# Optimization experiments

Measured on AMD Instinct MI355X. Metric: run time of the kernel, lower is better.

Reference implementation:

```python
import jax, jax.numpy as jnp
import numpy as np

N, E = 50000, 800000
NODE_IN, EDGE_IN = 32, 16
EMB, GEMB = 128, 128
H, C, L, B = 4, 32, 2, 8   # heads, per-head dim, layers, graphs
GAT_IN = NODE_IN + EMB      # skip_conn=True
NEG_SLOPE = 0.2
EPS = 1e-5


def layernorm(x, g, b):
    m = jnp.mean(x, -1, keepdims=True)
    v = jnp.mean((x - m) ** 2, -1, keepdims=True)
    return (x - m) / jnp.sqrt(v + EPS) * g + b


def setup_inputs() -> dict:
    key = jax.random.key(0)
    ks = jax.random.split(key, 24)
    s = 0.05
    return {
        "x": jax.random.normal(ks[0], (N, NODE_IN), jnp.float32),
        "edge_attr": jax.random.normal(ks[1], (E, EDGE_IN), jnp.float32),
        "W_in": jax.random.normal(ks[2], (NODE_IN, EMB), jnp.float32) * s,
        "b_in": jnp.zeros((EMB,), jnp.float32),
        "W_src": jax.random.normal(ks[3], (L, GAT_IN, H * C), jnp.float32) * s,
        "W_edge": jax.random.normal(ks[4], (L, EDGE_IN, H * C), jnp.float32) * s,
        "att_src": jax.random.normal(ks[5], (L, H, C), jnp.float32) * s,
        "att_dst": jax.random.normal(ks[6], (L, H, C), jnp.float32) * s,
        "att_edge": jax.random.normal(ks[7], (L, H, C), jnp.float32) * s,
        "gat_bias": jnp.zeros((L, H * C), jnp.float32),
        "ln_gamma": jnp.ones((L, EMB), jnp.float32),
        "ln_beta": jnp.zeros((L, EMB), jnp.float32),
        "W_out": jax.random.normal(ks[8], (EMB, EMB), jnp.float32) * s,
        "b_out": jnp.zeros((EMB,), jnp.float32),
        "ln_out_gamma": jnp.ones((EMB,), jnp.float32),
        "ln_out_beta": jnp.zeros((EMB,), jnp.float32),
        "W_g": jax.random.normal(ks[9], (EMB, GEMB), jnp.float32) * s,
        "b_g": jnp.zeros((GEMB,), jnp.float32),
        "g_gamma": jnp.ones((GEMB,), jnp.float32),
        "g_beta": jnp.zeros((GEMB,), jnp.float32),
        "edge_index": jax.random.randint(ks[10], (2, E), 0, N, jnp.int32),
        "batch": jnp.sort(jax.random.randint(ks[11], (N,), 0, B, jnp.int32)),
    }


def reference(x, edge_attr, W_in, b_in, W_src, W_edge, att_src, att_dst, att_edge,
              gat_bias, ln_gamma, ln_beta, W_out, b_out, ln_out_gamma, ln_out_beta,
              W_g, b_g, g_gamma, g_beta, edge_index, batch):
    # PyG GATConv adds self-loops with edge_attr fill_value='mean'
    loop = jnp.arange(N, dtype=edge_index.dtype)
    src = jnp.concatenate([edge_index[0], loop])   # [E2]
    dst = jnp.concatenate([edge_index[1], loop])   # [E2]
    ea = jnp.concatenate([edge_attr, jnp.broadcast_to(edge_attr.mean(0), (N, EDGE_IN))], 0)

    h = jax.nn.relu(x @ W_in + b_in)  # [N, EMB]
    for l in range(L):
        inp = jnp.concatenate([x, h], -1)                   # skip connection [N, GAT_IN]
        xs = (inp @ W_src[l]).reshape(N, H, C)              # projected nodes
        a_s = jnp.einsum('nhc,hc->nh', xs, att_src[l])
        a_d = jnp.einsum('nhc,hc->nh', xs, att_dst[l])
        ee = (ea @ W_edge[l]).reshape(-1, H, C)             # [E2, H, C]
        a_e = jnp.einsum('ehc,hc->eh', ee, att_edge[l])
        alpha = jax.nn.leaky_relu(a_s[src] + a_d[dst] + a_e, NEG_SLOPE)  # [E2, H]
        # segment softmax over incoming edges of each destination node
        amax = jax.ops.segment_max(alpha, dst, num_segments=N)
        ex = jnp.exp(alpha - amax[dst])
        denom = jax.ops.segment_sum(ex, dst, num_segments=N)
        w = ex / (denom[dst] + 1e-16)
        msg = xs[src] * w[:, :, None]                        # [E2, H, C]
        out = jax.ops.segment_sum(msg, dst, num_segments=N).reshape(N, H * C) + gat_bias[l]
        h = jax.nn.elu(layernorm(out, ln_gamma[l], ln_beta[l]))

    g = layernorm(jax.nn.relu(h @ W_g + b_g), g_gamma, g_beta)
    gsum = jax.ops.segment_sum(g, batch, num_segments=B)
    cnt = jax.ops.segment_sum(jnp.ones((N, 1), g.dtype), batch, num_segments=B)
    graph_embeddings = gsum / jnp.maximum(cnt, 1.0)

    node_embeddings = layernorm(jax.nn.relu(h @ W_out + b_out), ln_out_gamma, ln_out_beta)
    return node_embeddings, graph_embeddings
```

## Files before the change

kernel.cpp:

```cpp
#include <hip/hip_runtime.h>

#define N_NODES 50000
#define N_EDGES 800000
#define E2      850000
#define NODE_IN 32
#define EDGE_IN 16
#define EMB     128
#define GAT_IN  160
#define NLAYER  2
#define NGRAPH  8
#define NBLK    196
#define NB32    1563
#define NB64    782

#define GWT_SRC0 0
#define GWT_SRC1 20480
#define GWT_OUT  40960
#define GWT_G    57344
#define GWT_TOT  73728

typedef short bf16x8 __attribute__((ext_vector_type(8)));
typedef float f32x4 __attribute__((ext_vector_type(4)));

__device__ __forceinline__ unsigned int f2bf(float f) {
    unsigned int u = __float_as_uint(f);
    return (u + 0x7FFFu + ((u >> 16) & 1u)) >> 16;
}
__device__ __forceinline__ float bf2f(unsigned int h) {
    return __uint_as_float(h << 16);
}
__device__ __forceinline__ unsigned int pack2bf(float a, float b) {
    return f2bf(a) | (f2bf(b) << 16);
}

__global__ void zero_kernel(float* __restrict__ p, int n) {
    int i = blockIdx.x * blockDim.x + threadIdx.x;
    int stride = gridDim.x * blockDim.x;
    for (; i < n; i += stride) p[i] = 0.f;
}

__global__ __launch_bounds__(256) void count_mean_kernel(const int* __restrict__ edge_index,
                                                         const float* __restrict__ edge_attr,
                                                         int* __restrict__ cnt4,
                                                         int* __restrict__ rank,
                                                         float* __restrict__ meta) {
    __shared__ float sm[16];
    int t = threadIdx.x;
    int e = blockIdx.x * 256 + t;
    if (e < E2) {
        int dst = (e < N_EDGES) ? edge_index[N_EDGES + e] : (e - N_EDGES);
        int shard = blockIdx.x & 3;
        rank[e] = atomicAdd(&cnt4[shard * N_NODES + dst], 1);
    }
    if (blockIdx.x < 512) {
        if (t < 16) sm[t] = 0.f;
        __syncthreads();
        int gid = blockIdx.x * 256 + t;
        int q = gid & 3;
        const float4* ea4 = (const float4*)edge_attr;
        float4 s = make_float4(0.f, 0.f, 0.f, 0.f);
        for (int j = gid; j < N_EDGES * 4; j += 512 * 256) {
            float4 v = ea4[j];
            s.x += v.x; s.y += v.y; s.z += v.z; s.w += v.w;
        }
        atomicAdd(&sm[q * 4 + 0], s.x);
        atomicAdd(&sm[q * 4 + 1], s.y);
        atomicAdd(&sm[q * 4 + 2], s.z);
        atomicAdd(&sm[q * 4 + 3], s.w);
        __syncthreads();
        if (t < 16) atomicAdd(&meta[t], sm[t]);
    }
}

__global__ void prep_kernel(const float* __restrict__ W_edge,
                            const float* __restrict__ att_edge,
                            float* __restrict__ meta) {
    int t = threadIdx.x;
    if (t < EDGE_IN) meta[t] = meta[t] * (1.0f / (float)N_EDGES);
    __syncthreads();
    {
        int l = t >> 6, k = (t >> 2) & 15, h = t & 3;
        const float* w = W_edge + ((size_t)l * EDGE_IN + k) * EMB + h * 32;
        const float* a = att_edge + (size_t)l * EMB + h * 32;
        float acc = 0.f;
#pragma unroll
        for (int c = 0; c < 32; c++) acc += w[c] * a[c];
        meta[16 + (l * 16 + k) * 4 + h] = acc;
    }
    __syncthreads();
    if (t < 8) {
        int l = t >> 2, h = t & 3;
        float acc = 0.f;
#pragma unroll
        for (int k = 0; k < EDGE_IN; k++) acc += meta[k] * meta[16 + (l * 16 + k) * 4 + h];
        meta[144 + t] = acc;
    }
}

__global__ __launch_bounds__(256) void prep_wt_kernel(const float* __restrict__ Wsrc,
                                                      const float* __restrict__ Wout,
                                                      const float* __restrict__ Wg,
                                                      unsigned short* __restrict__ gwt) {
    int g = blockIdx.x * 256 + threadIdx.x;
    const float* Wm;
    int base, gg;
    if (g < 5120) {
        int l = g / 2560;
        gg = g - l * 2560;
        Wm = Wsrc + (size_t)l * GAT_IN * EMB;
        base = l * 20480;
    } else if (g < 7168) {
        gg = g - 5120;
        Wm = Wout;
        base = GWT_OUT;
    } else {
        gg = g - 7168;
        Wm = Wg;
        base = GWT_G;
    }
    int lane = gg & 63, tmp = gg >> 6;
    int nt = tmp & 7, kc = tmp >> 3;
    int quad = lane >> 4, l16 = lane & 15;
    int col = nt * 16 + l16, k0 = kc * 32 + quad * 8;
    unsigned int u[4];
#pragma unroll
    for (int j = 0; j < 4; j++)
        u[j] = pack2bf(Wm[(size_t)(k0 + 2 * j) * EMB + col], Wm[(size_t)(k0 + 2 * j + 1) * EMB + col]);
    *(uint4*)(gwt + base + (size_t)gg * 8) = make_uint4(u[0], u[1], u[2], u[3]);
}

__global__ __launch_bounds__(256) void scan1_kernel(const int* __restrict__ cnt4,
                                                    int* __restrict__ bsum) {
    __shared__ int sm[256];
    int t = threadIdx.x;
    int i = blockIdx.x * 256 + t;
    int tot = 0;
    if (i < N_NODES) {
#pragma unroll
        for (int s = 0; s < 4; s++) tot += cnt4[s * N_NODES + i];
    }
    sm[t] = tot;
    __syncthreads();
#pragma unroll
    for (int d = 128; d >= 1; d >>= 1) {
        if (t < d) sm[t] += sm[t + d];
        __syncthreads();
    }
    if (t == 0) bsum[blockIdx.x] = sm[0];
}

__global__ __launch_bounds__(256) void scan2_kernel(const int* __restrict__ bsum,
                                                    int* __restrict__ bbase) {
    __shared__ int sm[256];
    int t = threadIdx.x;
    int v = (t < NBLK) ? bsum[t] : 0;
    sm[t] = v;
    __syncthreads();
#pragma unroll
    for (int d = 1; d < 256; d <<= 1) {
        int u = (t >= d) ? sm[t - d] : 0;
        __syncthreads();
        sm[t] += u;
        __syncthreads();
    }
    if (t < NBLK) bbase[t] = sm[t] - v;
}

__global__ __launch_bounds__(256) void scan3_kernel(const int* __restrict__ bbase,
                                                    const int* __restrict__ cnt4,
                                                    int* __restrict__ off,
                                                    int* __restrict__ shard_base) {
    __shared__ int sm[256];
    int t = threadIdx.x;
    int i = blockIdx.x * 256 + t;
    int c[4] = {0, 0, 0, 0};
    int tot = 0;
    if (i < N_NODES) {
#pragma unroll
        for (int s = 0; s < 4; s++) {
            c[s] = cnt4[s * N_NODES + i];
            tot += c[s];
        }
    }
    sm[t] = tot;
    __syncthreads();
#pragma unroll
    for (int d = 1; d < 256; d <<= 1) {
        int u = (t >= d) ? sm[t - d] : 0;
        __syncthreads();
        sm[t] += u;
        __syncthreads();
    }
    if (i < N_NODES) {
        int base = bbase[blockIdx.x] + sm[t] - tot;
        off[i] = base;
        int4 sb;
        sb.x = base;            base += c[0];
        sb.y = base;            base += c[1];
        sb.z = base;            base += c[2];
        sb.w = base;
        *(int4*)(shard_base + i * 4) = sb;
        if (i == N_NODES - 1) off[N_NODES] = E2;
    }
}

__global__ __launch_bounds__(256) void fill_perm_kernel(const int* __restrict__ edge_index,
                                                        const int* __restrict__ rank,
                                                        const int* __restrict__ shard_base,
                                                        int* __restrict__ perm) {
    int e = blockIdx.x * 256 + threadIdx.x;
    if (e >= E2) return;
    int src, dst;
    if (e < N_EDGES) {
        src = edge_index[e];
        dst = edge_index[N_EDGES + e];
    } else {
        src = dst = e - N_EDGES;
    }
    int shard = (e >> 8) & 3;
    int pos = shard_base[dst * 4 + shard] + rank[e];
    ((int2*)perm)[pos] = make_int2(src, e);
}

__global__ __launch_bounds__(256) void compute_ae_kernel(const int* __restrict__ perm,
                                                         const float* __restrict__ edge_attr,
                                                         const float* __restrict__ meta,
                                                         int* __restrict__ csr_src,
                                                         float* __restrict__ csr_ae0,
                                                         float* __restrict__ csr_ae1) {
    __shared__ float Ml[128];
    __shared__ float loop_ae[8];
    int t = threadIdx.x;
    if (t < 128) Ml[t] = meta[16 + t];
    if (t < 8) loop_ae[t] = meta[144 + t];
    __syncthreads();
    int p = blockIdx.x * 256 + t;
    if (p >= E2) return;
    int2 pe = ((const int2*)perm)[p];
    int src = pe.x, e = pe.y;
    csr_src[p] = src;
    float ae[2][4];
    if (e < N_EDGES) {
        const float4* r4 = (const float4*)(edge_attr + (size_t)e * EDGE_IN);
#pragma unroll
        for (int l = 0; l < 2; l++)
#pragma unroll
            for (int hh = 0; hh < 4; hh++) ae[l][hh] = 0.f;
#pragma unroll
        for (int q = 0; q < 4; q++) {
            float4 v = r4[q];
#pragma unroll
            for (int l = 0; l < 2; l++) {
                const float* M = Ml + l * 64;
#pragma unroll
                for (int hh = 0; hh < 4; hh++) {
                    ae[l][hh] += v.x * M[(4 * q + 0) * 4 + hh] + v.y * M[(4 * q + 1) * 4 + hh] +
                                 v.z * M[(4 * q + 2) * 4 + hh] + v.w * M[(4 * q + 3) * 4 + hh];
                }
            }
        }
    } else {
#pragma unroll
        for (int l = 0; l < 2; l++)
#pragma unroll
            for (int hh = 0; hh < 4; hh++) ae[l][hh] = loop_ae[l * 4 + hh];
    }
    *(float4*)(csr_ae0 + (size_t)p * 4) = make_float4(ae[0][0], ae[0][1], ae[0][2], ae[0][3]);
    *(float4*)(csr_ae1 + (size_t)p * 4) = make_float4(ae[1][0], ae[1][1], ae[1][2], ae[1][3]);
}

__global__ __launch_bounds__(256) void input_proj_kernel(const float* __restrict__ x,
                                                         const float* __restrict__ W,
                                                         const float* __restrict__ b,
                                                         unsigned int* __restrict__ h_bf,
                                                         unsigned int* __restrict__ x_bf) {
    __shared__ float inp[32][NODE_IN];
    int t = threadIdx.x;
    int n0 = blockIdx.x * 32;
    for (int i = t; i < 32 * NODE_IN; i += 256) {
        int r = i >> 5, c = i & 31;
        int n = min(n0 + r, N_NODES - 1);
        inp[r][c] = x[(size_t)n * NODE_IN + c];
    }
    __syncthreads();
    for (int i = t; i < 32 * 16; i += 256) {
        int r = i >> 4, c = i & 15;
        int n = n0 + r;
        if (n < N_NODES) x_bf[(size_t)n * 16 + c] = pack2bf(inp[r][2 * c], inp[r][2 * c + 1]);
    }
    int wave = t >> 6, lane = t & 63;
    int c0 = lane * 2, c1 = c0 + 1;
    const float2* W2 = (const float2*)W;
    float acc[8][2];
#pragma unroll
    for (int j = 0; j < 8; j++) { acc[j][0] = b[c0]; acc[j][1] = b[c1]; }
#pragma unroll 2
    for (int k4 = 0; k4 < NODE_IN / 4; k4++) {
        float4 v[8];
#pragma unroll
        for (int j = 0; j < 8; j++) v[j] = *(const float4*)&inp[wave * 8 + j][k4 * 4];
#pragma unroll
        for (int kk = 0; kk < 4; kk++) {
            float2 w = W2[(k4 * 4 + kk) * 64 + lane];
#pragma unroll
            for (int j = 0; j < 8; j++) {
                float vv = (&v[j].x)[kk];
                acc[j][0] += vv * w.x;
                acc[j][1] += vv * w.y;
            }
        }
    }
#pragma unroll
    for (int j = 0; j < 8; j++) {
        int n = n0 + wave * 8 + j;
        if (n < N_NODES)
            h_bf[(size_t)n * 64 + lane] = pack2bf(fmaxf(acc[j][0], 0.f), fmaxf(acc[j][1], 0.f));
    }
}

template <int K, int MODE>
__global__ __launch_bounds__(256) void dense_mfma_kernel(
    const unsigned int* __restrict__ xbf, const unsigned int* __restrict__ hbf,
    const unsigned short* __restrict__ gwt, const float* __restrict__ bias,
    const float* __restrict__ v1, const float* __restrict__ v2,
    const int* __restrict__ batch,
    unsigned int* __restrict__ xs_out, float* __restrict__ a_s, float* __restrict__ a_d,
    float* __restrict__ out_nodes, float* __restrict__ gsum, float* __restrict__ gcnt) {
    constexpr int CLS = 132;
    __shared__ __align__(16) float cl[64 * CLS];
    __shared__ float red[(MODE != 0) ? 64 : 1][8];
    __shared__ float locw[(MODE == 2) ? 4 : 1][2][EMB];
    __shared__ int bids[(MODE == 2) ? 64 : 1];

    int t = threadIdx.x;
    int n0 = blockIdx.x * 64;
    if (MODE == 2 && t < 64) bids[t] = batch[min(n0 + t, N_NODES - 1)];

    int wave = t >> 6, lane = t & 63;
    int quad = lane >> 4, l16 = lane & 15;
    int arow = min(n0 + wave * 16 + l16, N_NODES - 1);
    const bf16x8* B = (const bf16x8*)gwt;
    f32x4 acc[8];
#pragma unroll
    for (int i = 0; i < 8; i++) acc[i] = (f32x4){0.f, 0.f, 0.f, 0.f};
#pragma unroll
    for (int kc = 0; kc < K / 32; kc++) {
        bf16x8 af;
        if (MODE == 0 && kc == 0) {
            af = *(const bf16x8*)(xbf + (size_t)arow * 16 + quad * 4);
        } else {
            int hk = ((MODE == 0) ? (kc - 1) : kc) * 16;
            af = *(const bf16x8*)(hbf + (size_t)arow * 64 + hk + quad * 4);
        }
#pragma unroll
        for (int nt = 0; nt < 8; nt++) {
            bf16x8 bfv = B[(kc * 8 + nt) * 64 + lane];
            acc[nt] = __builtin_amdgcn_mfma_f32_16x16x32_bf16(af, bfv, acc[nt], 0, 0, 0);
        }
    }
#pragma unroll
    for (int nt = 0; nt < 8; nt++) {
#pragma unroll
        for (int i = 0; i < 4; i++) {
            int r = wave * 16 + quad * 4 + i;
            cl[r * CLS + nt * 16 + l16] = acc[nt][i];
        }
    }
    __syncthreads();

    int p = t & 3, r = t >> 2;
    int n = n0 + r;
    const float4* c4 = (const float4*)(cl + r * CLS + p * 32);

    if (MODE == 0) {
        const float4* s4 = (const float4*)(v1 + p * 32);
        const float4* d4 = (const float4*)(v2 + p * 32);
        if (n < N_NODES) {
            float s_ = 0.f, d_ = 0.f;
#pragma unroll
            for (int i = 0; i < 8; i++) {
                float4 cv = c4[i], sv = s4[i], dv = d4[i];
                s_ += cv.x * sv.x + cv.y * sv.y + cv.z * sv.z + cv.w * sv.w;
                d_ += cv.x * dv.x + cv.y * dv.y + cv.z * dv.z + cv.w * dv.w;
                uint2 pk = make_uint2(pack2bf(cv.x, cv.y), pack2bf(cv.z, cv.w));
                *(uint2*)(xs_out + (size_t)n * 64 + p * 16 + 2 * i) = pk;
            }
            a_s[(size_t)n * 4 + p] = s_;
            a_d[(size_t)n * 4 + p] = d_;
        }
    } else {
        const float4* b4 = (const float4*)(bias + p * 32);
        float vals[32];
        float s_ = 0.f, q_ = 0.f;
#pragma unroll
        for (int i = 0; i < 8; i++) {
            float4 cv = c4[i], bv = b4[i];
            float w0 = fmaxf(cv.x + bv.x, 0.f), w1 = fmaxf(cv.y + bv.y, 0.f);
            float w2 = fmaxf(cv.z + bv.z, 0.f), w3 = fmaxf(cv.w + bv.w, 0.f);
            vals[4 * i] = w0; vals[4 * i + 1] = w1; vals[4 * i + 2] = w2; vals[4 * i + 3] = w3;
            s_ += w0 + w1 + w2 + w3;
            q_ += w0 * w0 + w1 * w1 + w2 * w2 + w3 * w3;
        }
        red[r][p] = s_;
        red[r][4 + p] = q_;
        __syncthreads();
        float sm = red[r][0] + red[r][1] + red[r][2] + red[r][3];
        float sq = red[r][4] + red[r][5] + red[r][6] + red[r][7];
        float mean = sm * (1.f / EMB);
        float var = sq * (1.f / EMB) - mean * mean;
        float rstd = rsqrtf(var + 1e-5f);
        const float4* g4 = (const float4*)(v1 + p * 32);
        const float4* be4 = (const float4*)(v2 + p * 32);
#pragma unroll
        for (int i = 0; i < 8; i++) {
            float4 gv = g4[i], bv = be4[i];
            vals[4 * i]     = (vals[4 * i]     - mean) * rstd * gv.x + bv.x;
            vals[4 * i + 1] = (vals[4 * i + 1] - mean) * rstd * gv.y + bv.y;
            vals[4 * i + 2] = (vals[4 * i + 2] - mean) * rstd * gv.z + bv.z;
            vals[4 * i + 3] = (vals[4 * i + 3] - mean) * rstd * gv.w + bv.w;
        }
        if (MODE == 1) {
            if (n < N_NODES) {
                float* op = out_nodes + (size_t)n * EMB + p * 32;
#pragma unroll
                for (int i = 0; i < 8; i++)
                    *(float4*)(op + 4 * i) = make_float4(vals[4 * i], vals[4 * i + 1],
                                                         vals[4 * i + 2], vals[4 * i + 3]);
            }
        } else {
            int nvalid = min(64, N_NODES - n0);
            int bmin = bids[0], bmax = bids[nvalid - 1];
            int bid = bids[r];
            bool inA = (bid == bmin) && (n < N_NODES);
            bool inB = (bid == bmax) && (bmax != bmin) && (n < N_NODES);
            if (n < N_NODES && bid != bmin && bid != bmax) {
#pragma unroll
                for (int i = 0; i < 32; i++)
                    atomicAdd(&gsum[(size_t)bid * EMB + p * 32 + i], vals[i]);
            }
#pragma unroll
            for (int g = 0; g < 2; g++) {
                bool m = g ? inB : inA;
#pragma unroll
                for (int i = 0; i < 32; i++) {
                    float v = m ? vals[i] : 0.f;
                    v += __shfl_xor(v, 4, 64);
                    v += __shfl_xor(v, 8, 64);
                    v += __shfl_xor(v, 16, 64);
                    v += __shfl_xor(v, 32, 64);
                    if ((lane >> 2) == 0) locw[wave][g][(lane & 3) * 32 + i] = v;
                }
            }
            __syncthreads();
            if (t < 128) {
                float sA = locw[0][0][t] + locw[1][0][t] + locw[2][0][t] + locw[3][0][t];
                atomicAdd(&gsum[(size_t)bmin * EMB + t], sA);
                if (bmax != bmin) {
                    float sB = locw[0][1][t] + locw[1][1][t] + locw[2][1][t] + locw[3][1][t];
                    atomicAdd(&gsum[(size_t)bmax * EMB + t], sB);
                }
            } else if (t == 255) {
                int cA = 0, cB = 0;
                for (int rr = 0; rr < nvalid; rr++) {
                    int bb = bids[rr];
                    if (bb == bmin) cA++;
                    else if (bb == bmax) cB++;
                    else atomicAdd(&gcnt[bb], 1.f);
                }
                atomicAdd(&gcnt[bmin], (float)cA);
                if (bmax != bmin && cB > 0) atomicAdd(&gcnt[bmax], (float)cB);
            }
        }
    }
}

__global__ __launch_bounds__(256) void gat_gather_kernel(const int* __restrict__ off,
                                                         const int* __restrict__ csr_src,
                                                         const float* __restrict__ csr_ae,
                                                         const unsigned int* __restrict__ xs,
                                                         const float* __restrict__ a_s,
                                                         const float* __restrict__ a_d,
                                                         const float* __restrict__ bias_l,
                                                         const float* __restrict__ gamma_l,
                                                         const float* __restrict__ beta_l,
                                                         unsigned int* __restrict__ h_bf) {
    int t = threadIdx.x, wave = t >> 6, lane = t & 63;
    int n = blockIdx.x * 4 + wave;
    int g = lane >> 4, l16 = lane & 15;
    int h = l16 >> 2;
    float ad = a_d[(size_t)n * 4 + h];
    int p0 = __builtin_amdgcn_readfirstlane(off[n]);
    int p1 = __builtin_amdgcn_readfirstlane(off[n + 1]);
    int plast = p1 - 1;
    float den = 0.f;
    float acc[8];
#pragma unroll
    for (int j = 0; j < 8; j++) acc[j] = 0.f;

    for (int pb = p0; pb < p1; pb += 8) {
        int pA = pb + g, pB = pb + 4 + g;
        int iA = min(pA, plast), iB = min(pB, plast);
        int sA = csr_src[iA], sB = csr_src[iB];
        float aeA = csr_ae[(size_t)iA * 4 + h];
        float aeB = csr_ae[(size_t)iB * 4 + h];
        float asA = a_s[(size_t)sA * 4 + h];
        float asB = a_s[(size_t)sB * 4 + h];
        uint4 xA = *(const uint4*)(xs + (size_t)sA * 64 + l16 * 4);
        uint4 xB = *(const uint4*)(xs + (size_t)sB * 64 + l16 * 4);
        float alA = asA + ad + aeA;
        alA = alA > 0.f ? alA : 0.2f * alA;
        float exA = (pA <= plast) ? __expf(alA) : 0.f;
        float alB = asB + ad + aeB;
        alB = alB > 0.f ? alB : 0.2f * alB;
        float exB = (pB <= plast) ? __expf(alB) : 0.f;
        den += exA + exB;
        unsigned int u;
        u = xA.x; acc[0] += exA * bf2f(u & 0xFFFFu); acc[1] += exA * bf2f(u >> 16);
        u = xA.y; acc[2] += exA * bf2f(u & 0xFFFFu); acc[3] += exA * bf2f(u >> 16);
        u = xA.z; acc[4] += exA * bf2f(u & 0xFFFFu); acc[5] += exA * bf2f(u >> 16);
        u = xA.w; acc[6] += exA * bf2f(u & 0xFFFFu); acc[7] += exA * bf2f(u >> 16);
        u = xB.x; acc[0] += exB * bf2f(u & 0xFFFFu); acc[1] += exB * bf2f(u >> 16);
        u = xB.y; acc[2] += exB * bf2f(u & 0xFFFFu); acc[3] += exB * bf2f(u >> 16);
        u = xB.z; acc[4] += exB * bf2f(u & 0xFFFFu); acc[5] += exB * bf2f(u >> 16);
        u = xB.w; acc[6] += exB * bf2f(u & 0xFFFFu); acc[7] += exB * bf2f(u >> 16);
    }
#pragma unroll
    for (int j = 0; j < 8; j++) {
        acc[j] += __shfl_xor(acc[j], 16, 64);
        acc[j] += __shfl_xor(acc[j], 32, 64);
    }
    den += __shfl_xor(den, 16, 64);
    den += __shfl_xor(den, 32, 64);

    float dinv = 1.0f / (den + 1e-16f);
    int c0 = l16 * 8;
    const float4* b4 = (const float4*)(bias_l + c0);
    float4 bv0 = b4[0], bv1 = b4[1];
    float v[8];
    v[0] = acc[0] * dinv + bv0.x; v[1] = acc[1] * dinv + bv0.y;
    v[2] = acc[2] * dinv + bv0.z; v[3] = acc[3] * dinv + bv0.w;
    v[4] = acc[4] * dinv + bv1.x; v[5] = acc[5] * dinv + bv1.y;
    v[6] = acc[6] * dinv + bv1.z; v[7] = acc[7] * dinv + bv1.w;
    float sm = 0.f, sq = 0.f;
#pragma unroll
    for (int j = 0; j < 8; j++) { sm += v[j]; sq += v[j] * v[j]; }
#pragma unroll
    for (int o = 1; o <= 8; o <<= 1) {
        sm += __shfl_xor(sm, o, 64);
        sq += __shfl_xor(sq, o, 64);
    }
    float mean = sm * (1.f / EMB);
    float var = sq * (1.f / EMB) - mean * mean;
    float rstd = rsqrtf(var + 1e-5f);
    const float4* g4 = (const float4*)(gamma_l + c0);
    const float4* be4 = (const float4*)(beta_l + c0);
    float4 gv0 = g4[0], gv1 = g4[1], bev0 = be4[0], bev1 = be4[1];
    float y[8];
    y[0] = (v[0] - mean) * rstd * gv0.x + bev0.x;
    y[1] = (v[1] - mean) * rstd * gv0.y + bev0.y;
    y[2] = (v[2] - mean) * rstd * gv0.z + bev0.z;
    y[3] = (v[3] - mean) * rstd * gv0.w + bev0.w;
    y[4] = (v[4] - mean) * rstd * gv1.x + bev1.x;
    y[5] = (v[5] - mean) * rstd * gv1.y + bev1.y;
    y[6] = (v[6] - mean) * rstd * gv1.z + bev1.z;
    y[7] = (v[7] - mean) * rstd * gv1.w + bev1.w;
#pragma unroll
    for (int j = 0; j < 8; j++) y[j] = y[j] > 0.f ? y[j] : __expf(y[j]) - 1.f;
    if (g == 0) {
        uint4 o4;
        o4.x = pack2bf(y[0], y[1]);
        o4.y = pack2bf(y[2], y[3]);
        o4.z = pack2bf(y[4], y[5]);
        o4.w = pack2bf(y[6], y[7]);
        *(uint4*)(h_bf + (size_t)n * 64 + l16 * 4) = o4;
    }
}

__global__ void graph_out_kernel(const float* __restrict__ gsum, const float* __restrict__ gcnt,
                                 float* __restrict__ out) {
    int i = blockIdx.x * blockDim.x + threadIdx.x;
    if (i >= NGRAPH * EMB) return;
    int b = i >> 7;
    float c = fmaxf(gcnt[b], 1.f);
    out[(size_t)N_NODES * EMB + i] = gsum[i] / c;
}

extern "C" void kernel_launch(void* const* d_in, const int* in_sizes, int n_in,
                              void* d_out, int out_size, void* d_ws, size_t ws_size,
                              hipStream_t stream) {
    (void)in_sizes; (void)n_in; (void)out_size; (void)ws_size;
    const float* x         = (const float*)d_in[0];
    const float* edge_attr = (const float*)d_in[1];
    const float* W_in      = (const float*)d_in[2];
    const float* b_in      = (const float*)d_in[3];
    const float* W_src     = (const float*)d_in[4];
    const float* W_edge    = (const float*)d_in[5];
    const float* att_src   = (const float*)d_in[6];
    const float* att_dst   = (const float*)d_in[7];
    const float* att_edge  = (const float*)d_in[8];
    const float* gat_bias  = (const float*)d_in[9];
    const float* ln_gamma  = (const float*)d_in[10];
    const float* ln_beta   = (const float*)d_in[11];
    const float* W_out     = (const float*)d_in[12];
    const float* b_out     = (const float*)d_in[13];
    const float* ln_og     = (const float*)d_in[14];
    const float* ln_ob     = (const float*)d_in[15];
    const float* W_g       = (const float*)d_in[16];
    const float* b_g       = (const float*)d_in[17];
    const float* g_gamma   = (const float*)d_in[18];
    const float* g_beta    = (const float*)d_in[19];
    const int* edge_index  = (const int*)d_in[20];
    const int* batch       = (const int*)d_in[21];
    float* out = (float*)d_out;

    float* ws              = (float*)d_ws;
    unsigned int* h_bf     = (unsigned int*)ws;
    unsigned int* xs       = h_bf + (size_t)N_NODES * 64;
    unsigned int* x_bf     = xs + (size_t)N_NODES * 64;
    float* a_s             = (float*)(x_bf + (size_t)N_NODES * 16);
    float* a_d             = a_s + (size_t)N_NODES * 4;
    float* csr_ae          = a_d + (size_t)N_NODES * 4;
    unsigned short* gwt    = (unsigned short*)(csr_ae + (size_t)2 * E2 * 4);
    float* meta            = (float*)(gwt + GWT_TOT);
    float* gsum            = meta + 152;
    float* gcnt            = gsum + NGRAPH * EMB;
    int*   cnt4            = (int*)(gcnt + NGRAPH);
    int*   off             = cnt4 + 4 * N_NODES;
    int*   shard_base      = off + N_NODES + 1;
    int*   rank            = shard_base + 4 * N_NODES;
    int*   csr_src         = rank + E2;
    int*   bsum            = csr_src + E2;
    int*   bbase           = bsum + NBLK;
    int*   perm            = (int*)xs;

    const int EB = (E2 + 255) / 256;

    zero_kernel<<<256, 256, 0, stream>>>(meta, 152 + NGRAPH * EMB + NGRAPH + 4 * N_NODES);
    count_mean_kernel<<<EB, 256, 0, stream>>>(edge_index, edge_attr, cnt4, rank, meta);
    prep_kernel<<<1, 128, 0, stream>>>(W_edge, att_edge, meta);
    prep_wt_kernel<<<36, 256, 0, stream>>>(W_src, W_out, W_g, gwt);
    input_proj_kernel<<<NB32, 256, 0, stream>>>(x, W_in, b_in, h_bf, x_bf);

    scan1_kernel<<<NBLK, 256, 0, stream>>>(cnt4, bsum);
    scan2_kernel<<<1, 256, 0, stream>>>(bsum, bbase);
    scan3_kernel<<<NBLK, 256, 0, stream>>>(bbase, cnt4, off, shard_base);
    fill_perm_kernel<<<EB, 256, 0, stream>>>(edge_index, rank, shard_base, perm);
    compute_ae_kernel<<<EB, 256, 0, stream>>>(perm, edge_attr, meta,
                                              csr_src, csr_ae, csr_ae + (size_t)E2 * 4);

    for (int l = 0; l < NLAYER; l++) {
        dense_mfma_kernel<GAT_IN, 0><<<NB64, 256, 0, stream>>>(
            x_bf, h_bf, gwt + (l ? GWT_SRC1 : GWT_SRC0), nullptr,
            att_src + (size_t)l * EMB, att_dst + (size_t)l * EMB, nullptr,
            xs, a_s, a_d, nullptr, nullptr, nullptr);
        gat_gather_kernel<<<N_NODES / 4, 256, 0, stream>>>(
            off, csr_src, csr_ae + (size_t)l * E2 * 4, xs, a_s, a_d,
            gat_bias + (size_t)l * EMB, ln_gamma + (size_t)l * EMB,
            ln_beta + (size_t)l * EMB, h_bf);
    }

    dense_mfma_kernel<EMB, 1><<<NB64, 256, 0, stream>>>(
        nullptr, h_bf, gwt + GWT_OUT, b_out, ln_og, ln_ob, nullptr,
        nullptr, nullptr, nullptr, out, nullptr, nullptr);
    dense_mfma_kernel<EMB, 2><<<NB64, 256, 0, stream>>>(
        nullptr, h_bf, gwt + GWT_G, b_g, g_gamma, g_beta, batch,
        nullptr, nullptr, nullptr, nullptr, gsum, gcnt);
    graph_out_kernel<<<4, 256, 0, stream>>>(gsum, gcnt, out);
}
```

Baseline: 432.6 us.

## Merge preprocessing kernels into one launch and widen degree-count sharding to 8

Combines the edge degree counting and edge_attr mean reduction, the input projection, and the weight bf16 repacking into a single block-partitioned kernel. The edge-attention prep work moves into the scan2 kernel, which removes several launches and lets independent preprocessing stages run concurrently. The per-destination atomic counters go from 4 to 8 shards to reduce atomic contention. In exchange, the scan and fill kernels read twice as many counter arrays, and the workspace layout grows.

```diff
diff --git a/kernel.cpp b/kernel.cpp
--- a/kernel.cpp
+++ b/kernel.cpp
@@ -12,6 +12,7 @@
 #define NBLK    196
 #define NB32    1563
 #define NB64    782
+#define EB      3321
 
 #define GWT_SRC0 0
 #define GWT_SRC1 20480
@@ -39,97 +40,117 @@
     for (; i < n; i += stride) p[i] = 0.f;
 }
 
-__global__ __launch_bounds__(256) void count_mean_kernel(const int* __restrict__ edge_index,
-                                                         const float* __restrict__ edge_attr,
-                                                         int* __restrict__ cnt4,
-                                                         int* __restrict__ rank,
-                                                         float* __restrict__ meta) {
-    __shared__ float sm[16];
-    int t = threadIdx.x;
-    int e = blockIdx.x * 256 + t;
-    if (e < E2) {
-        int dst = (e < N_EDGES) ? edge_index[N_EDGES + e] : (e - N_EDGES);
-        int shard = blockIdx.x & 3;
-        rank[e] = atomicAdd(&cnt4[shard * N_NODES + dst], 1);
-    }
-    if (blockIdx.x < 512) {
-        if (t < 16) sm[t] = 0.f;
+__global__ __launch_bounds__(256) void mega_kernel(
+    const int* __restrict__ edge_index, const float* __restrict__ edge_attr,
+    const float* __restrict__ x, const float* __restrict__ W_in,
+    const float* __restrict__ b_in,
+    const float* __restrict__ Wsrc, const float* __restrict__ Wout,
+    const float* __restrict__ Wg,
+    int* __restrict__ cnt8, int* __restrict__ rank, float* __restrict__ meta,
+    unsigned int* __restrict__ h_bf, unsigned int* __restrict__ x_bf,
+    unsigned short* __restrict__ gwt) {
+    __shared__ float smem[32 * NODE_IN];
+    int b = blockIdx.x, t = threadIdx.x;
+
+    if (b < EB) {
+        int e = b * 256 + t;
+        if (e < E2) {
+            int dst = (e < N_EDGES) ? edge_index[N_EDGES + e] : (e - N_EDGES);
+            int shard = b & 7;
+            rank[e] = atomicAdd(&cnt8[shard * N_NODES + dst], 1);
+        }
+        if (b < 512) {
+            if (t < 16) smem[t] = 0.f;
+            __syncthreads();
+            int gid = b * 256 + t;
+            int q = gid & 3;
+            const float4* ea4 = (const float4*)edge_attr;
+            float4 s = make_float4(0.f, 0.f, 0.f, 0.f);
+            for (int j = gid; j < N_EDGES * 4; j += 512 * 256) {
+                float4 v = ea4[j];
+                s.x += v.x; s.y += v.y; s.z += v.z; s.w += v.w;
+            }
+            atomicAdd(&smem[q * 4 + 0], s.x);
+            atomicAdd(&smem[q * 4 + 1], s.y);
+            atomicAdd(&smem[q * 4 + 2], s.z);
+            atomicAdd(&smem[q * 4 + 3], s.w);
+            __syncthreads();
+            if (t < 16) atomicAdd(&meta[t], smem[t]);
+        }
+    } else if (b < EB + NB32) {
+        float (*inp)[NODE_IN] = (float (*)[NODE_IN])smem;
+        int n0 = (b - EB) * 32;
+        for (int i = t; i < 32 * NODE_IN; i += 256) {
+            int r = i >> 5, c = i & 31;
+            int n = min(n0 + r, N_NODES - 1);
+            inp[r][c] = x[(size_t)n * NODE_IN + c];
+        }
         __syncthreads();
-        int gid = blockIdx.x * 256 + t;
-        int q = gid & 3;
-        const float4* ea4 = (const float4*)edge_attr;
-        float4 s = make_float4(0.f, 0.f, 0.f, 0.f);
-        for (int j = gid; j < N_EDGES * 4; j += 512 * 256) {
-            float4 v = ea4[j];
-            s.x += v.x; s.y += v.y; s.z += v.z; s.w += v.w;
-        }
-        atomicAdd(&sm[q * 4 + 0], s.x);
-        atomicAdd(&sm[q * 4 + 1], s.y);
-        atomicAdd(&sm[q * 4 + 2], s.z);
-        atomicAdd(&sm[q * 4 + 3], s.w);
-        __syncthreads();
-        if (t < 16) atomicAdd(&meta[t], sm[t]);
-    }
-}
-
-__global__ void prep_kernel(const float* __restrict__ W_edge,
-                            const float* __restrict__ att_edge,
-                            float* __restrict__ meta) {
-    int t = threadIdx.x;
-    if (t < EDGE_IN) meta[t] = meta[t] * (1.0f / (float)N_EDGES);
-    __syncthreads();
-    {
-        int l = t >> 6, k = (t >> 2) & 15, h = t & 3;
-        const float* w = W_edge + ((size_t)l * EDGE_IN + k) * EMB + h * 32;
-        const float* a = att_edge + (size_t)l * EMB + h * 32;
-        float acc = 0.f;
-#pragma unroll
-        for (int c = 0; c < 32; c++) acc += w[c] * a[c];
-        meta[16 + (l * 16 + k) * 4 + h] = acc;
-    }
-    __syncthreads();
-    if (t < 8) {
-        int l = t >> 2, h = t & 3;
-        float acc = 0.f;
-#pragma unroll
-        for (int k = 0; k < EDGE_IN; k++) acc += meta[k] * meta[16 + (l * 16 + k) * 4 + h];
-        meta[144 + t] = acc;
-    }
-}
-
-__global__ __launch_bounds__(256) void prep_wt_kernel(const float* __restrict__ Wsrc,
-                                                      const float* __restrict__ Wout,
-                                                      const float* __restrict__ Wg,
-                                                      unsigned short* __restrict__ gwt) {
-    int g = blockIdx.x * 256 + threadIdx.x;
-    const float* Wm;
-    int base, gg;
-    if (g < 5120) {
-        int l = g / 2560;
-        gg = g - l * 2560;
-        Wm = Wsrc + (size_t)l * GAT_IN * EMB;
-        base = l * 20480;
-    } else if (g < 7168) {
-        gg = g - 5120;
-        Wm = Wout;
-        base = GWT_OUT;
+        for (int i = t; i < 32 * 16; i += 256) {
+            int r = i >> 4, c = i & 15;
+            int n = n0 + r;
+            if (n < N_NODES) x_bf[(size_t)n * 16 + c] = pack2bf(inp[r][2 * c], inp[r][2 * c + 1]);
+        }
+        int wave = t >> 6, lane = t & 63;
+        int c0 = lane * 2, c1 = c0 + 1;
+        const float2* W2 = (const float2*)W_in;
+        float acc[8][2];
+#pragma unroll
+        for (int j = 0; j < 8; j++) { acc[j][0] = b_in[c0]; acc[j][1] = b_in[c1]; }
+#pragma unroll 2
+        for (int k4 = 0; k4 < NODE_IN / 4; k4++) {
+            float4 v[8];
+#pragma unroll
+            for (int j = 0; j < 8; j++) v[j] = *(const float4*)&inp[wave * 8 + j][k4 * 4];
+#pragma unroll
+            for (int kk = 0; kk < 4; kk++) {
+                float2 w = W2[(k4 * 4 + kk) * 64 + lane];
+#pragma unroll
+                for (int j = 0; j < 8; j++) {
+                    float vv = (&v[j].x)[kk];
+                    acc[j][0] += vv * w.x;
+                    acc[j][1] += vv * w.y;
+                }
+            }
+        }
+#pragma unroll
+        for (int j = 0; j < 8; j++) {
+            int n = n0 + wave * 8 + j;
+            if (n < N_NODES)
+                h_bf[(size_t)n * 64 + lane] = pack2bf(fmaxf(acc[j][0], 0.f), fmaxf(acc[j][1], 0.f));
+        }
     } else {
-        gg = g - 7168;
-        Wm = Wg;
-        base = GWT_G;
-    }
-    int lane = gg & 63, tmp = gg >> 6;
-    int nt = tmp & 7, kc = tmp >> 3;
-    int quad = lane >> 4, l16 = lane & 15;
-    int col = nt * 16 + l16, k0 = kc * 32 + quad * 8;
-    unsigned int u[4];
-#pragma unroll
-    for (int j = 0; j < 4; j++)
-        u[j] = pack2bf(Wm[(size_t)(k0 + 2 * j) * EMB + col], Wm[(size_t)(k0 + 2 * j + 1) * EMB + col]);
-    *(uint4*)(gwt + base + (size_t)gg * 8) = make_uint4(u[0], u[1], u[2], u[3]);
-}
-
-__global__ __launch_bounds__(256) void scan1_kernel(const int* __restrict__ cnt4,
+        int g = (b - EB - NB32) * 256 + t;
+        const float* Wm;
+        int base, gg;
+        if (g < 5120) {
+            int l = g / 2560;
+            gg = g - l * 2560;
+            Wm = Wsrc + (size_t)l * GAT_IN * EMB;
+            base = l * 20480;
+        } else if (g < 7168) {
+            gg = g - 5120;
+            Wm = Wout;
+            base = GWT_OUT;
+        } else {
+            gg = g - 7168;
+            Wm = Wg;
+            base = GWT_G;
+        }
+        int lane = gg & 63, tmp = gg >> 6;
+        int nt = tmp & 7, kc = tmp >> 3;
+        int quad = lane >> 4, l16 = lane & 15;
+        int col = nt * 16 + l16, k0 = kc * 32 + quad * 8;
+        unsigned int u[4];
+#pragma unroll
+        for (int j = 0; j < 4; j++)
+            u[j] = pack2bf(Wm[(size_t)(k0 + 2 * j) * EMB + col],
+                           Wm[(size_t)(k0 + 2 * j + 1) * EMB + col]);
+        *(uint4*)(gwt + base + (size_t)gg * 8) = make_uint4(u[0], u[1], u[2], u[3]);
+    }
+}
+
+__global__ __launch_bounds__(256) void scan1_kernel(const int* __restrict__ cnt8,
                                                     int* __restrict__ bsum) {
     __shared__ int sm[256];
     int t = threadIdx.x;
@@ -137,7 +158,7 @@
     int tot = 0;
     if (i < N_NODES) {
 #pragma unroll
-        for (int s = 0; s < 4; s++) tot += cnt4[s * N_NODES + i];
+        for (int s = 0; s < 8; s++) tot += cnt8[s * N_NODES + i];
     }
     sm[t] = tot;
     __syncthreads();
@@ -149,8 +170,11 @@
     if (t == 0) bsum[blockIdx.x] = sm[0];
 }
 
-__global__ __launch_bounds__(256) void scan2_kernel(const int* __restrict__ bsum,
-                                                    int* __restrict__ bbase) {
+__global__ __launch_bounds__(256) void scan2_prep_kernel(const int* __restrict__ bsum,
+                                                         int* __restrict__ bbase,
+                                                         const float* __restrict__ W_edge,
+                                                         const float* __restrict__ att_edge,
+                                                         float* __restrict__ meta) {
     __shared__ int sm[256];
     int t = threadIdx.x;
     int v = (t < NBLK) ? bsum[t] : 0;
@@ -164,21 +188,41 @@
         __syncthreads();
     }
     if (t < NBLK) bbase[t] = sm[t] - v;
+
+    if (t < EDGE_IN) meta[t] = meta[t] * (1.0f / (float)N_EDGES);
+    __syncthreads();
+    if (t < 128) {
+        int l = t >> 6, k = (t >> 2) & 15, h = t & 3;
+        const float* w = W_edge + ((size_t)l * EDGE_IN + k) * EMB + h * 32;
+        const float* a = att_edge + (size_t)l * EMB + h * 32;
+        float acc = 0.f;
+#pragma unroll
+        for (int c = 0; c < 32; c++) acc += w[c] * a[c];
+        meta[16 + (l * 16 + k) * 4 + h] = acc;
+    }
+    __syncthreads();
+    if (t < 8) {
+        int l = t >> 2, h = t & 3;
+        float acc = 0.f;
+#pragma unroll
+        for (int k = 0; k < EDGE_IN; k++) acc += meta[k] * meta[16 + (l * 16 + k) * 4 + h];
+        meta[144 + t] = acc;
+    }
 }
 
 __global__ __launch_bounds__(256) void scan3_kernel(const int* __restrict__ bbase,
-                                                    const int* __restrict__ cnt4,
+                                                    const int* __restrict__ cnt8,
                                                     int* __restrict__ off,
                                                     int* __restrict__ shard_base) {
     __shared__ int sm[256];
     int t = threadIdx.x;
     int i = blockIdx.x * 256 + t;
-    int c[4] = {0, 0, 0, 0};
+    int c[8] = {0, 0, 0, 0, 0, 0, 0, 0};
     int tot = 0;
     if (i < N_NODES) {
 #pragma unroll
-        for (int s = 0; s < 4; s++) {
-            c[s] = cnt4[s * N_NODES + i];
+        for (int s = 0; s < 8; s++) {
+            c[s] = cnt8[s * N_NODES + i];
             tot += c[s];
         }
     }
@@ -194,12 +238,17 @@
     if (i < N_NODES) {
         int base = bbase[blockIdx.x] + sm[t] - tot;
         off[i] = base;
-        int4 sb;
-        sb.x = base;            base += c[0];
-        sb.y = base;            base += c[1];
-        sb.z = base;            base += c[2];
-        sb.w = base;
-        *(int4*)(shard_base + i * 4) = sb;
+        int4 sb0, sb1;
+        sb0.x = base;           base += c[0];
+        sb0.y = base;           base += c[1];
+        sb0.z = base;           base += c[2];
+        sb0.w = base;           base += c[3];
+        sb1.x = base;           base += c[4];
+        sb1.y = base;           base += c[5];
+        sb1.z = base;           base += c[6];
+        sb1.w = base;
+        *(int4*)(shard_base + (size_t)i * 8) = sb0;
+        *(int4*)(shard_base + (size_t)i * 8 + 4) = sb1;
         if (i == N_NODES - 1) off[N_NODES] = E2;
     }
 }
@@ -217,8 +266,8 @@
     } else {
         src = dst = e - N_EDGES;
     }
-    int shard = (e >> 8) & 3;
-    int pos = shard_base[dst * 4 + shard] + rank[e];
+    int shard = (e >> 8) & 7;
+    int pos = shard_base[(size_t)dst * 8 + shard] + rank[e];
     ((int2*)perm)[pos] = make_int2(src, e);
 }
 
@@ -267,55 +316,6 @@
     }
     *(float4*)(csr_ae0 + (size_t)p * 4) = make_float4(ae[0][0], ae[0][1], ae[0][2], ae[0][3]);
     *(float4*)(csr_ae1 + (size_t)p * 4) = make_float4(ae[1][0], ae[1][1], ae[1][2], ae[1][3]);
-}
-
-__global__ __launch_bounds__(256) void input_proj_kernel(const float* __restrict__ x,
-                                                         const float* __restrict__ W,
-                                                         const float* __restrict__ b,
-                                                         unsigned int* __restrict__ h_bf,
-                                                         unsigned int* __restrict__ x_bf) {
-    __shared__ float inp[32][NODE_IN];
-    int t = threadIdx.x;
-    int n0 = blockIdx.x * 32;
-    for (int i = t; i < 32 * NODE_IN; i += 256) {
-        int r = i >> 5, c = i & 31;
-        int n = min(n0 + r, N_NODES - 1);
-        inp[r][c] = x[(size_t)n * NODE_IN + c];
-    }
-    __syncthreads();
-    for (int i = t; i < 32 * 16; i += 256) {
-        int r = i >> 4, c = i & 15;
-        int n = n0 + r;
-        if (n < N_NODES) x_bf[(size_t)n * 16 + c] = pack2bf(inp[r][2 * c], inp[r][2 * c + 1]);
-    }
-    int wave = t >> 6, lane = t & 63;
-    int c0 = lane * 2, c1 = c0 + 1;
-    const float2* W2 = (const float2*)W;
-    float acc[8][2];
-#pragma unroll
-    for (int j = 0; j < 8; j++) { acc[j][0] = b[c0]; acc[j][1] = b[c1]; }
-#pragma unroll 2
-    for (int k4 = 0; k4 < NODE_IN / 4; k4++) {
-        float4 v[8];
-#pragma unroll
-        for (int j = 0; j < 8; j++) v[j] = *(const float4*)&inp[wave * 8 + j][k4 * 4];
-#pragma unroll
-        for (int kk = 0; kk < 4; kk++) {
-            float2 w = W2[(k4 * 4 + kk) * 64 + lane];
-#pragma unroll
-            for (int j = 0; j < 8; j++) {
-                float vv = (&v[j].x)[kk];
-                acc[j][0] += vv * w.x;
-                acc[j][1] += vv * w.y;
-            }
-        }
-    }
-#pragma unroll
-    for (int j = 0; j < 8; j++) {
-        int n = n0 + wave * 8 + j;
-        if (n < N_NODES)
-            h_bf[(size_t)n * 64 + lane] = pack2bf(fmaxf(acc[j][0], 0.f), fmaxf(acc[j][1], 0.f));
-    }
 }
 
 template <int K, int MODE>
@@ -624,26 +624,23 @@
     float* meta            = (float*)(gwt + GWT_TOT);
     float* gsum            = meta + 152;
     float* gcnt            = gsum + NGRAPH * EMB;
-    int*   cnt4            = (int*)(gcnt + NGRAPH);
-    int*   off             = cnt4 + 4 * N_NODES;
+    int*   cnt8            = (int*)(gcnt + NGRAPH);
+    int*   off             = cnt8 + 8 * N_NODES;
     int*   shard_base      = off + N_NODES + 1;
-    int*   rank            = shard_base + 4 * N_NODES;
+    int*   rank            = shard_base + 8 * N_NODES;
     int*   csr_src         = rank + E2;
     int*   bsum            = csr_src + E2;
     int*   bbase           = bsum + NBLK;
     int*   perm            = (int*)xs;
 
-    const int EB = (E2 + 255) / 256;
-
-    zero_kernel<<<256, 256, 0, stream>>>(meta, 152 + NGRAPH * EMB + NGRAPH + 4 * N_NODES);
-    count_mean_kernel<<<EB, 256, 0, stream>>>(edge_index, edge_attr, cnt4, rank, meta);
-    prep_kernel<<<1, 128, 0, stream>>>(W_edge, att_edge, meta);
-    prep_wt_kernel<<<36, 256, 0, stream>>>(W_src, W_out, W_g, gwt);
-    input_proj_kernel<<<NB32, 256, 0, stream>>>(x, W_in, b_in, h_bf, x_bf);
-
-    scan1_kernel<<<NBLK, 256, 0, stream>>>(cnt4, bsum);
-    scan2_kernel<<<1, 256, 0, stream>>>(bsum, bbase);
-    scan3_kernel<<<NBLK, 256, 0, stream>>>(bbase, cnt4, off, shard_base);
+    zero_kernel<<<256, 256, 0, stream>>>(meta, 152 + NGRAPH * EMB + NGRAPH + 8 * N_NODES);
+    mega_kernel<<<EB + NB32 + 36, 256, 0, stream>>>(
+        edge_index, edge_attr, x, W_in, b_in, W_src, W_out, W_g,
+        cnt8, rank, meta, h_bf, x_bf, gwt);
+
+    scan1_kernel<<<NBLK, 256, 0, stream>>>(cnt8, bsum);
+    scan2_prep_kernel<<<1, 256, 0, stream>>>(bsum, bbase, W_edge, att_edge, meta);
+    scan3_kernel<<<NBLK, 256, 0, stream>>>(bbase, cnt8, off, shard_base);
     fill_perm_kernel<<<EB, 256, 0, stream>>>(edge_index, rank, shard_base, perm);
     compute_ae_kernel<<<EB, 256, 0, stream>>>(perm, edge_attr, meta,
                                               csr_src, csr_ae, csr_ae + (size_t)E2 * 4);
```

After: 421.8 us. 1.03x faster.
